# Optimization experiments

Measured on AMD Instinct MI355X. Metric: run time of the kernel, lower is better.

Reference implementation:

```python
import jax, jax.numpy as jnp
import numpy as np

N = 50000
E = 1600000
IN_DIM = 128
H = 8
D = 16  # out_dim per head


def setup_inputs() -> dict:
    key = jax.random.key(0)
    ks = jax.random.split(key, 9)
    h = jax.random.normal(ks[0], (N, IN_DIM), dtype=jnp.float32)
    src = jax.random.randint(ks[1], (E,), 0, N, dtype=jnp.int32)
    dst = jax.random.randint(ks[2], (E,), 0, N, dtype=jnp.int32)
    s = 1.0 / np.sqrt(IN_DIM)
    WQ = jax.random.uniform(ks[3], (IN_DIM, H * D), jnp.float32, -s, s)
    WK = jax.random.uniform(ks[4], (IN_DIM, H * D), jnp.float32, -s, s)
    WV = jax.random.uniform(ks[5], (IN_DIM, H * D), jnp.float32, -s, s)
    bQ = jax.random.uniform(ks[6], (H * D,), jnp.float32, -s, s)
    bK = jax.random.uniform(ks[7], (H * D,), jnp.float32, -s, s)
    bV = jax.random.uniform(ks[8], (H * D,), jnp.float32, -s, s)
    return {"h": h, "src": src, "dst": dst, "WQ": WQ, "WK": WK, "WV": WV,
            "bQ": bQ, "bK": bK, "bV": bV}


def reference(h, src, dst, WQ, WK, WV, bQ, bK, bV):
    # Node projections -> [N, H, D]
    Q = (h @ WQ + bQ).reshape(-1, H, D)
    K = (h @ WK + bK).reshape(-1, H, D)
    V = (h @ WV + bV).reshape(-1, H, D)
    # Edge scores: dot(K[src], Q[dst]) per head, scaled+clamped exp -> [E, H]
    scale = jnp.float32(np.sqrt(D))
    score = jnp.exp(jnp.clip(jnp.sum(K[src] * Q[dst], axis=-1) / scale, -5.0, 5.0))
    # Scatter-sum to destination nodes
    wV = jax.ops.segment_sum(score[:, :, None] * V[src], dst, num_segments=N)  # [N, H, D]
    z = jax.ops.segment_sum(score, dst, num_segments=N)  # [N, H]
    return wV / z[:, :, None]
```

## Files before the change

kernel.cpp:

```cpp
#include <hip/hip_runtime.h>

#define N_NODES 50000
#define N_PAD   50048
#define N_EDGES 1600000
#define HD 128
#define CHUNK 2048
#define NCHUNK ((N_EDGES + CHUNK - 1) / CHUNK)
#define NBUCKET ((N_NODES + 127) / 128)

typedef __attribute__((ext_vector_type(8))) short short8;
typedef __attribute__((ext_vector_type(4))) float floatx4;

union U4S8 { uint4 u; short8 s; };

__device__ __forceinline__ unsigned short f2bf(float f) {
    unsigned u = __float_as_uint(f);
    unsigned r = (u + 0x7fffu + ((u >> 16) & 1u)) >> 16;
    return (unsigned short)r;
}

#define HB_BLOCKS ((N_PAD * HD / 8) / 256)

__global__ __launch_bounds__(256) void prep_kernel(
    const float* __restrict__ h,
    const float* __restrict__ WQ, const float* __restrict__ WK, const float* __restrict__ WV,
    unsigned short* __restrict__ hb, unsigned short* __restrict__ Wf) {
    int bid = blockIdx.x, t = threadIdx.x;
    if (bid < HB_BLOCKS) {
        int tid = bid * 256 + t;
        int row = tid >> 4, c8 = tid & 15;
        uint4 outv;
        if (row < N_NODES) {
            const float4* src = (const float4*)(h + (size_t)row * HD + c8 * 8);
            float4 a = src[0], b = src[1];
            unsigned short r[8];
            r[0] = f2bf(a.x); r[1] = f2bf(a.y);
            r[2] = f2bf(a.z); r[3] = f2bf(a.w);
            r[4] = f2bf(b.x); r[5] = f2bf(b.y);
            r[6] = f2bf(b.z); r[7] = f2bf(b.w);
            outv = *(uint4*)r;
        } else {
            outv = make_uint4(0, 0, 0, 0);
        }
        *(uint4*)(hb + (size_t)tid * 8) = outv;
    } else {
        int tid = (bid - HB_BLOCKS) * 256 + t;
        if (tid < 24 * 4 * 64) {
            int lane = tid & 63;
            int kstep = (tid >> 6) & 3;
            int ntile = tid >> 8;
            int g = ntile >> 3;
            int c = (ntile & 7) * 16 + (lane & 15);
            int k0 = kstep * 32 + (lane >> 4) * 8;
            const float* W = (g == 0) ? WQ : (g == 1) ? WK : WV;
            unsigned short r[8];
#pragma unroll
            for (int j = 0; j < 8; ++j)
                r[j] = f2bf(W[(size_t)(k0 + j) * HD + c]);
            *(uint4*)(Wf + (size_t)tid * 8) = *(uint4*)r;
        }
    }
}


__global__ __launch_bounds__(256) void k_chunkhist(const int* __restrict__ dst,
                                                   int* __restrict__ chunkhist,
                                                   int* __restrict__ btot) {
    __shared__ int hist[NBUCKET];
    int t = threadIdx.x, c = blockIdx.x;
    for (int i = t; i < NBUCKET; i += 256) hist[i] = 0;
    __syncthreads();
    int e0 = c * CHUNK;
    int cnt = min(CHUNK, N_EDGES - e0);
    for (int i = t; i < cnt; i += 256)
        atomicAdd(&hist[dst[e0 + i] >> 7], 1);
    __syncthreads();
    for (int i = t; i < NBUCKET; i += 256) {
        int v = hist[i];
        chunkhist[c * NBUCKET + i] = v;
        if (v) atomicAdd(&btot[i], v);
    }
}

__global__ __launch_bounds__(512) void k_bscan(const int* __restrict__ btot,
                                               int* __restrict__ bucket_ptr) {
    int t = threadIdx.x;
    int v = (t < NBUCKET) ? btot[t] : 0;
    __shared__ int part[512];
    part[t] = v;
    __syncthreads();
    for (int off = 1; off < 512; off <<= 1) {
        int x = (t >= off) ? part[t - off] : 0;
        __syncthreads();
        part[t] += x;
        __syncthreads();
    }
    if (t < NBUCKET) bucket_ptr[t] = part[t] - v;
    if (t == NBUCKET - 1) bucket_ptr[NBUCKET] = part[t];
}

__global__ __launch_bounds__(256) void k_choff(const int* __restrict__ chunkhist,
                                               const int* __restrict__ bucket_ptr,
                                               int* __restrict__ chunkoff) {
    const int PER = (NCHUNK + 255) / 256;
    int b = blockIdx.x, t = threadIdx.x;
    int c0 = t * PER;
    int v[PER];
    int s = 0;
#pragma unroll
    for (int i = 0; i < PER; ++i) {
        int c = c0 + i;
        v[i] = (c < NCHUNK) ? chunkhist[c * NBUCKET + b] : 0;
        s += v[i];
    }
    __shared__ int part[256];
    part[t] = s;
    __syncthreads();
    for (int off = 1; off < 256; off <<= 1) {
        int x = (t >= off) ? part[t - off] : 0;
        __syncthreads();
        part[t] += x;
        __syncthreads();
    }
    int run = bucket_ptr[b] + part[t] - s;
#pragma unroll
    for (int i = 0; i < PER; ++i) {
        int c = c0 + i;
        if (c < NCHUNK) { chunkoff[c * NBUCKET + b] = run; run += v[i]; }
    }
}

__global__ __launch_bounds__(256) void k_scatter(const int* __restrict__ src,
                                                 const int* __restrict__ dst,
                                                 const int* __restrict__ chunkoff,
                                                 int* __restrict__ packed) {
    __shared__ int cur[NBUCKET];
    int t = threadIdx.x, c = blockIdx.x;
    for (int i = t; i < NBUCKET; i += 256) cur[i] = chunkoff[c * NBUCKET + i];
    __syncthreads();
    int e0 = c * CHUNK;
    int cnt = min(CHUNK, N_EDGES - e0);
    for (int i = t; i < cnt; i += 256) {
        int d = dst[e0 + i], s = src[e0 + i];
        int pos = atomicAdd(&cur[d >> 7], 1);
        packed[pos] = (s << 7) | (d & 127);
    }
}

__global__ __launch_bounds__(256) void k_finalize(const int* __restrict__ bucket_ptr,
                                                  const int* __restrict__ packed,
                                                  int* __restrict__ row_ptr,
                                                  int* __restrict__ col_src) {
    __shared__ int hist[128], part[128], cur[128];
    int b = blockIdx.x, t = threadIdx.x;
    if (t < 128) hist[t] = 0;
    __syncthreads();
    int ebeg = bucket_ptr[b], eend = bucket_ptr[b + 1];
    int m = eend - ebeg;
    for (int i = t; i < m; i += 256)
        atomicAdd(&hist[packed[ebeg + i] & 127], 1);
    __syncthreads();
    int v = 0;
    if (t < 128) { v = hist[t]; part[t] = v; }
    __syncthreads();
    for (int off = 1; off < 128; off <<= 1) {
        int x = 0;
        if (t < 128 && t >= off) x = part[t - off];
        __syncthreads();
        if (t < 128) part[t] += x;
        __syncthreads();
    }
    if (t < 128) {
        int excl = part[t] - v;
        int node = b * 128 + t;
        if (node < N_NODES) row_ptr[node] = ebeg + excl;
        if (node == N_NODES - 1) row_ptr[N_NODES] = eend;
        cur[t] = ebeg + excl;
    }
    __syncthreads();
    for (int i = t; i < m; i += 256) {
        int p = packed[ebeg + i];
        int pos = atomicAdd(&cur[p & 127], 1);
        col_src[pos] = p >> 7;
    }
}


__global__ __launch_bounds__(256) void proj_mfma(
    const unsigned short* __restrict__ hb, const unsigned short* __restrict__ Wf,
    const float* __restrict__ bQ, const float* __restrict__ bK, const float* __restrict__ bV,
    float* __restrict__ Qo, unsigned short* __restrict__ Kb, unsigned short* __restrict__ Vb) {
    int t = threadIdx.x;
    int w = t >> 6;
    int l = t & 63;
    int m0 = blockIdx.x * 64;
    int nt0 = w * 6;

    floatx4 acc[4][6];
#pragma unroll
    for (int mt = 0; mt < 4; ++mt)
#pragma unroll
        for (int nt = 0; nt < 6; ++nt)
            acc[mt][nt] = (floatx4){0.f, 0.f, 0.f, 0.f};

    int arow = m0 + (l & 15);
    int akoff = (l >> 4) * 8;

#pragma unroll
    for (int kstep = 0; kstep < 4; ++kstep) {
        short8 a[4], b[6];
#pragma unroll
        for (int mt = 0; mt < 4; ++mt) {
            U4S8 u;
            u.u = *(const uint4*)(hb + (size_t)(arow + mt * 16) * HD + akoff + kstep * 32);
            a[mt] = u.s;
        }
#pragma unroll
        for (int nt = 0; nt < 6; ++nt) {
            U4S8 u;
            u.u = *(const uint4*)(Wf + ((size_t)((nt0 + nt) * 4 + kstep) * 64 + l) * 8);
            b[nt] = u.s;
        }
#pragma unroll
        for (int mt = 0; mt < 4; ++mt)
#pragma unroll
            for (int nt = 0; nt < 6; ++nt)
                acc[mt][nt] = __builtin_amdgcn_mfma_f32_16x16x32_bf16(
                    a[mt], b[nt], acc[mt][nt], 0, 0, 0);
    }

#pragma unroll
    for (int nt = 0; nt < 6; ++nt) {
        int ntile = nt0 + nt;
        int g = ntile >> 3;
        int cc = (ntile & 7) * 16 + (l & 15);
        float bias = (g == 0) ? bQ[cc] : (g == 1) ? bK[cc] : bV[cc];
#pragma unroll
        for (int mt = 0; mt < 4; ++mt) {
#pragma unroll
            for (int r = 0; r < 4; ++r) {
                int grow = m0 + mt * 16 + (l >> 4) * 4 + r;
                if (grow < N_NODES) {
                    float val = acc[mt][nt][r] + bias;
                    if (g == 0)      Qo[(size_t)grow * HD + cc] = val;
                    else if (g == 1) Kb[(size_t)grow * HD + cc] = f2bf(val);
                    else             Vb[(size_t)grow * HD + cc] = f2bf(val);
                }
            }
        }
    }
}


__device__ __forceinline__ float blo(unsigned u) { return __uint_as_float(u << 16); }
__device__ __forceinline__ float bhi(unsigned u) { return __uint_as_float(u & 0xffff0000u); }

__global__ __launch_bounds__(64) void attn_kernel(
    const float* __restrict__ Q,
    const unsigned short* __restrict__ Kb, const unsigned short* __restrict__ Vb,
    const int* __restrict__ row_ptr, const int* __restrict__ col_src,
    float* __restrict__ out) {
    int n = blockIdx.x;
    int t = threadIdx.x;
    int o = t >> 3;
    int p = t & 7;

    const float4* Qv = (const float4*)(Q + (size_t)n * HD + p * 16);
    float4 q0 = Qv[0], q1 = Qv[1], q2 = Qv[2], q3 = Qv[3];

    float acc[16];
#pragma unroll
    for (int j = 0; j < 16; ++j) acc[j] = 0.f;
    float z = 0.f;

    int beg = row_ptr[n], end = row_ptr[n + 1];

    for (int base = beg; base < end; base += 64) {
        int mm = min(64, end - base);
        int e_l = col_src[(base + t < end) ? (base + t) : beg];
        int steps = (mm + 7) >> 3;

        int s0 = __shfl(e_l, o);
        const uint4* Kp = (const uint4*)(Kb + (size_t)s0 * HD + p * 16);
        const uint4* Vp = (const uint4*)(Vb + (size_t)s0 * HD + p * 16);
        uint4 ka = Kp[0], kb = Kp[1], va = Vp[0], vb = Vp[1];

        for (int i = 0; i < steps; ++i) {
            uint4 nka = ka, nkb = kb, nva = va, nvb = vb;
            if (i + 1 < steps) {
                int s1 = __shfl(e_l, 8 * (i + 1) + o);
                const uint4* Kn = (const uint4*)(Kb + (size_t)s1 * HD + p * 16);
                const uint4* Vn = (const uint4*)(Vb + (size_t)s1 * HD + p * 16);
                nka = Kn[0]; nkb = Kn[1]; nva = Vn[0]; nvb = Vn[1];
            }
            float dot = blo(ka.x) * q0.x + bhi(ka.x) * q0.y
                      + blo(ka.y) * q0.z + bhi(ka.y) * q0.w
                      + blo(ka.z) * q1.x + bhi(ka.z) * q1.y
                      + blo(ka.w) * q1.z + bhi(ka.w) * q1.w
                      + blo(kb.x) * q2.x + bhi(kb.x) * q2.y
                      + blo(kb.y) * q2.z + bhi(kb.y) * q2.w
                      + blo(kb.z) * q3.x + bhi(kb.z) * q3.y
                      + blo(kb.w) * q3.z + bhi(kb.w) * q3.w;
            float sc = __expf(fminf(fmaxf(dot * 0.25f, -5.f), 5.f));
            if (8 * i + o >= mm) sc = 0.f;
            acc[0]  = fmaf(sc, blo(va.x), acc[0]);
            acc[1]  = fmaf(sc, bhi(va.x), acc[1]);
            acc[2]  = fmaf(sc, blo(va.y), acc[2]);
            acc[3]  = fmaf(sc, bhi(va.y), acc[3]);
            acc[4]  = fmaf(sc, blo(va.z), acc[4]);
            acc[5]  = fmaf(sc, bhi(va.z), acc[5]);
            acc[6]  = fmaf(sc, blo(va.w), acc[6]);
            acc[7]  = fmaf(sc, bhi(va.w), acc[7]);
            acc[8]  = fmaf(sc, blo(vb.x), acc[8]);
            acc[9]  = fmaf(sc, bhi(vb.x), acc[9]);
            acc[10] = fmaf(sc, blo(vb.y), acc[10]);
            acc[11] = fmaf(sc, bhi(vb.y), acc[11]);
            acc[12] = fmaf(sc, blo(vb.z), acc[12]);
            acc[13] = fmaf(sc, bhi(vb.z), acc[13]);
            acc[14] = fmaf(sc, blo(vb.w), acc[14]);
            acc[15] = fmaf(sc, bhi(vb.w), acc[15]);
            z += sc;
            ka = nka; kb = nkb; va = nva; vb = nvb;
        }
    }

#pragma unroll
    for (int j = 0; j < 16; ++j) {
        acc[j] += __shfl_xor(acc[j], 8);
        acc[j] += __shfl_xor(acc[j], 16);
        acc[j] += __shfl_xor(acc[j], 32);
    }
    z += __shfl_xor(z, 8);
    z += __shfl_xor(z, 16);
    z += __shfl_xor(z, 32);

    if (o == 0) {
        float inv = 1.f / z;
        float4* O = (float4*)(out + (size_t)n * HD + p * 16);
        O[0] = (float4){acc[0] * inv,  acc[1] * inv,  acc[2] * inv,  acc[3] * inv};
        O[1] = (float4){acc[4] * inv,  acc[5] * inv,  acc[6] * inv,  acc[7] * inv};
        O[2] = (float4){acc[8] * inv,  acc[9] * inv,  acc[10] * inv, acc[11] * inv};
        O[3] = (float4){acc[12] * inv, acc[13] * inv, acc[14] * inv, acc[15] * inv};
    }
}


static inline char* align256(char* p) {
    return (char*)(((uintptr_t)p + 255) & ~(uintptr_t)255);
}

extern "C" void kernel_launch(void* const* d_in, const int* in_sizes, int n_in,
                              void* d_out, int out_size, void* d_ws, size_t ws_size,
                              hipStream_t stream) {
    const float* h  = (const float*)d_in[0];
    const int*   src = (const int*)d_in[1];
    const int*   dst = (const int*)d_in[2];
    const float* WQ = (const float*)d_in[3];
    const float* WK = (const float*)d_in[4];
    const float* WV = (const float*)d_in[5];
    const float* bQ = (const float*)d_in[6];
    const float* bK = (const float*)d_in[7];
    const float* bV = (const float*)d_in[8];
    float* out = (float*)d_out;

    char* p = (char*)d_ws;
    float* Q = (float*)p;                 p += (size_t)N_PAD * HD * 4;
    unsigned short* Kb = (unsigned short*)p; p += (size_t)N_PAD * HD * 2;
    unsigned short* Vb = (unsigned short*)p; p += (size_t)N_PAD * HD * 2;
    unsigned short* hb = (unsigned short*)p; p += (size_t)N_PAD * HD * 2;
    unsigned short* Wf = (unsigned short*)p; p += (size_t)24 * 4 * 64 * 8 * 2;
    p = align256(p);
    int* row_ptr    = (int*)p;            p += (N_NODES + 2) * 4;
    p = align256(p);
    int* bucket_ptr = (int*)p;            p += (NBUCKET + 1) * 4;
    p = align256(p);
    int* btot       = (int*)p;            p += NBUCKET * 4;
    p = align256(p);
    int* chunkhist  = (int*)p;            p += (size_t)NCHUNK * NBUCKET * 4;
    p = align256(p);
    int* chunkoff   = (int*)p;            p += (size_t)NCHUNK * NBUCKET * 4;
    p = align256(p);
    int* packed     = (int*)p;            p += (size_t)N_EDGES * 4;
    p = align256(p);
    int* col_src    = (int*)p;            p += (size_t)N_EDGES * 4;

    (void)hipMemsetAsync(btot, 0, NBUCKET * sizeof(int), stream);
    prep_kernel<<<HB_BLOCKS + 24, 256, 0, stream>>>(h, WQ, WK, WV, hb, Wf);
    k_chunkhist<<<NCHUNK, 256, 0, stream>>>(dst, chunkhist, btot);
    k_bscan<<<1, 512, 0, stream>>>(btot, bucket_ptr);
    k_choff<<<NBUCKET, 256, 0, stream>>>(chunkhist, bucket_ptr, chunkoff);
    k_scatter<<<NCHUNK, 256, 0, stream>>>(src, dst, chunkoff, packed);
    k_finalize<<<NBUCKET, 256, 0, stream>>>(bucket_ptr, packed, row_ptr, col_src);
    proj_mfma<<<N_PAD / 64, 256, 0, stream>>>(hb, Wf, bQ, bK, bV, Q, Kb, Vb);
    attn_kernel<<<N_NODES, 64, 0, stream>>>(Q, Kb, Vb, row_ptr, col_src, out);
}
```

Before: 307.0 us.

## Fuse bf16 conversion into projection, merge scan kernels, vectorize edge sorting

```diff
diff --git a/kernel.cpp b/kernel.cpp
--- a/kernel.cpp
+++ b/kernel.cpp
@@ -4,7 +4,7 @@
 #define N_PAD   50048
 #define N_EDGES 1600000
 #define HD 128
-#define CHUNK 2048
+#define CHUNK 4096
 #define NCHUNK ((N_EDGES + CHUNK - 1) / CHUNK)
 #define NBUCKET ((N_NODES + 127) / 128)
 
@@ -19,46 +19,27 @@
     return (unsigned short)r;
 }
 
-#define HB_BLOCKS ((N_PAD * HD / 8) / 256)
-
 __global__ __launch_bounds__(256) void prep_kernel(
-    const float* __restrict__ h,
     const float* __restrict__ WQ, const float* __restrict__ WK, const float* __restrict__ WV,
-    unsigned short* __restrict__ hb, unsigned short* __restrict__ Wf) {
+    unsigned short* __restrict__ Wf, int* __restrict__ btot) {
     int bid = blockIdx.x, t = threadIdx.x;
-    if (bid < HB_BLOCKS) {
+    if (bid < 24) {
         int tid = bid * 256 + t;
-        int row = tid >> 4, c8 = tid & 15;
-        uint4 outv;
-        if (row < N_NODES) {
-            const float4* src = (const float4*)(h + (size_t)row * HD + c8 * 8);
-            float4 a = src[0], b = src[1];
-            unsigned short r[8];
-            r[0] = f2bf(a.x); r[1] = f2bf(a.y);
-            r[2] = f2bf(a.z); r[3] = f2bf(a.w);
-            r[4] = f2bf(b.x); r[5] = f2bf(b.y);
-            r[6] = f2bf(b.z); r[7] = f2bf(b.w);
-            outv = *(uint4*)r;
-        } else {
-            outv = make_uint4(0, 0, 0, 0);
-        }
-        *(uint4*)(hb + (size_t)tid * 8) = outv;
+        int lane = tid & 63;
+        int kstep = (tid >> 6) & 3;
+        int ntile = tid >> 8;
+        int g = ntile >> 3;
+        int c = (ntile & 7) * 16 + (lane & 15);
+        int k0 = kstep * 32 + (lane >> 4) * 8;
+        const float* W = (g == 0) ? WQ : (g == 1) ? WK : WV;
+        unsigned short r[8];
+#pragma unroll
+        for (int j = 0; j < 8; ++j)
+            r[j] = f2bf(W[(size_t)(k0 + j) * HD + c]);
+        *(uint4*)(Wf + (size_t)tid * 8) = *(uint4*)r;
     } else {
-        int tid = (bid - HB_BLOCKS) * 256 + t;
-        if (tid < 24 * 4 * 64) {
-            int lane = tid & 63;
-            int kstep = (tid >> 6) & 3;
-            int ntile = tid >> 8;
-            int g = ntile >> 3;
-            int c = (ntile & 7) * 16 + (lane & 15);
-            int k0 = kstep * 32 + (lane >> 4) * 8;
-            const float* W = (g == 0) ? WQ : (g == 1) ? WK : WV;
-            unsigned short r[8];
-#pragma unroll
-            for (int j = 0; j < 8; ++j)
-                r[j] = f2bf(W[(size_t)(k0 + j) * HD + c]);
-            *(uint4*)(Wf + (size_t)tid * 8) = *(uint4*)r;
-        }
+        int i = (bid - 24) * 256 + t;
+        if (i < NBUCKET) btot[i] = 0;
     }
 }
 
@@ -72,8 +53,15 @@
     __syncthreads();
     int e0 = c * CHUNK;
     int cnt = min(CHUNK, N_EDGES - e0);
-    for (int i = t; i < cnt; i += 256)
-        atomicAdd(&hist[dst[e0 + i] >> 7], 1);
+    const uint4* d4 = (const uint4*)(dst + e0);
+    int cnt4 = cnt >> 2;
+    for (int i = t; i < cnt4; i += 256) {
+        uint4 v = d4[i];
+        atomicAdd(&hist[v.x >> 7], 1);
+        atomicAdd(&hist[v.y >> 7], 1);
+        atomicAdd(&hist[v.z >> 7], 1);
+        atomicAdd(&hist[v.w >> 7], 1);
+    }
     __syncthreads();
     for (int i = t; i < NBUCKET; i += 256) {
         int v = hist[i];
@@ -82,28 +70,27 @@
     }
 }
 
-__global__ __launch_bounds__(512) void k_bscan(const int* __restrict__ btot,
-                                               int* __restrict__ bucket_ptr) {
-    int t = threadIdx.x;
-    int v = (t < NBUCKET) ? btot[t] : 0;
-    __shared__ int part[512];
-    part[t] = v;
-    __syncthreads();
-    for (int off = 1; off < 512; off <<= 1) {
-        int x = (t >= off) ? part[t - off] : 0;
-        __syncthreads();
-        part[t] += x;
-        __syncthreads();
-    }
-    if (t < NBUCKET) bucket_ptr[t] = part[t] - v;
-    if (t == NBUCKET - 1) bucket_ptr[NBUCKET] = part[t];
-}
-
 __global__ __launch_bounds__(256) void k_choff(const int* __restrict__ chunkhist,
-                                               const int* __restrict__ bucket_ptr,
+                                               const int* __restrict__ btot,
+                                               int* __restrict__ bucket_ptr,
                                                int* __restrict__ chunkoff) {
+    int b = blockIdx.x, t = threadIdx.x;
+    int x = 0;
+    for (int i = t; i < NBUCKET; i += 256)
+        if (i < b) x += btot[i];
+    __shared__ int red[256];
+    red[t] = x;
+    __syncthreads();
+    for (int off = 128; off > 0; off >>= 1) {
+        if (t < off) red[t] += red[t + off];
+        __syncthreads();
+    }
+    int base = red[0];
+    if (t == 0) {
+        bucket_ptr[b] = base;
+        if (b == NBUCKET - 1) bucket_ptr[NBUCKET] = base + btot[b];
+    }
     const int PER = (NCHUNK + 255) / 256;
-    int b = blockIdx.x, t = threadIdx.x;
     int c0 = t * PER;
     int v[PER];
     int s = 0;
@@ -117,12 +104,12 @@
     part[t] = s;
     __syncthreads();
     for (int off = 1; off < 256; off <<= 1) {
-        int x = (t >= off) ? part[t - off] : 0;
-        __syncthreads();
-        part[t] += x;
-        __syncthreads();
-    }
-    int run = bucket_ptr[b] + part[t] - s;
+        int y = (t >= off) ? part[t - off] : 0;
+        __syncthreads();
+        part[t] += y;
+        __syncthreads();
+    }
+    int run = base + part[t] - s;
 #pragma unroll
     for (int i = 0; i < PER; ++i) {
         int c = c0 + i;
@@ -140,10 +127,17 @@
     __syncthreads();
     int e0 = c * CHUNK;
     int cnt = min(CHUNK, N_EDGES - e0);
-    for (int i = t; i < cnt; i += 256) {
-        int d = dst[e0 + i], s = src[e0 + i];
-        int pos = atomicAdd(&cur[d >> 7], 1);
-        packed[pos] = (s << 7) | (d & 127);
+    const uint4* d4 = (const uint4*)(dst + e0);
+    const uint4* s4 = (const uint4*)(src + e0);
+    int cnt4 = cnt >> 2;
+    for (int i = t; i < cnt4; i += 256) {
+        uint4 d = d4[i];
+        uint4 s = s4[i];
+        int pos;
+        pos = atomicAdd(&cur[d.x >> 7], 1); packed[pos] = (s.x << 7) | (d.x & 127);
+        pos = atomicAdd(&cur[d.y >> 7], 1); packed[pos] = (s.y << 7) | (d.y & 127);
+        pos = atomicAdd(&cur[d.z >> 7], 1); packed[pos] = (s.z << 7) | (d.z & 127);
+        pos = atomicAdd(&cur[d.w >> 7], 1); packed[pos] = (s.w << 7) | (d.w & 127);
     }
 }
 
@@ -187,7 +181,7 @@
 
 
 __global__ __launch_bounds__(256) void proj_mfma(
-    const unsigned short* __restrict__ hb, const unsigned short* __restrict__ Wf,
+    const float* __restrict__ h, const unsigned short* __restrict__ Wf,
     const float* __restrict__ bQ, const float* __restrict__ bK, const float* __restrict__ bV,
     float* __restrict__ Qo, unsigned short* __restrict__ Kb, unsigned short* __restrict__ Vb) {
     int t = threadIdx.x;
@@ -211,9 +205,18 @@
         short8 a[4], b[6];
 #pragma unroll
         for (int mt = 0; mt < 4; ++mt) {
-            U4S8 u;
-            u.u = *(const uint4*)(hb + (size_t)(arow + mt * 16) * HD + akoff + kstep * 32);
-            a[mt] = u.s;
+            int row = arow + mt * 16;
+            unsigned short r[8];
+            if (row < N_NODES) {
+                const float4* ap = (const float4*)(h + (size_t)row * HD + akoff + kstep * 32);
+                float4 f0 = ap[0], f1 = ap[1];
+                r[0] = f2bf(f0.x); r[1] = f2bf(f0.y); r[2] = f2bf(f0.z); r[3] = f2bf(f0.w);
+                r[4] = f2bf(f1.x); r[5] = f2bf(f1.y); r[6] = f2bf(f1.z); r[7] = f2bf(f1.w);
+            } else {
+#pragma unroll
+                for (int j = 0; j < 8; ++j) r[j] = 0;
+            }
+            a[mt] = *(short8*)r;
         }
 #pragma unroll
         for (int nt = 0; nt < 6; ++nt) {
@@ -255,15 +258,16 @@
 __device__ __forceinline__ float blo(unsigned u) { return __uint_as_float(u << 16); }
 __device__ __forceinline__ float bhi(unsigned u) { return __uint_as_float(u & 0xffff0000u); }
 
-__global__ __launch_bounds__(64) void attn_kernel(
+__global__ __launch_bounds__(256) void attn_kernel(
     const float* __restrict__ Q,
     const unsigned short* __restrict__ Kb, const unsigned short* __restrict__ Vb,
     const int* __restrict__ row_ptr, const int* __restrict__ col_src,
     float* __restrict__ out) {
-    int n = blockIdx.x;
-    int t = threadIdx.x;
-    int o = t >> 3;
-    int p = t & 7;
+    int n = blockIdx.x * 4 + (threadIdx.x >> 6);
+    if (n >= N_NODES) return;
+    int l = threadIdx.x & 63;
+    int o = l >> 3;
+    int p = l & 7;
 
     const float4* Qv = (const float4*)(Q + (size_t)n * HD + p * 16);
     float4 q0 = Qv[0], q1 = Qv[1], q2 = Qv[2], q3 = Qv[3];
@@ -277,7 +281,7 @@
 
     for (int base = beg; base < end; base += 64) {
         int mm = min(64, end - base);
-        int e_l = col_src[(base + t < end) ? (base + t) : beg];
+        int e_l = col_src[(base + l < end) ? (base + l) : beg];
         int steps = (mm + 7) >> 3;
 
         int s0 = __shfl(e_l, o);
@@ -364,33 +368,30 @@
     float* out = (float*)d_out;
 
     char* p = (char*)d_ws;
-    float* Q = (float*)p;                 p += (size_t)N_PAD * HD * 4;
+    float* Q = (float*)p;                    p += (size_t)N_PAD * HD * 4;
     unsigned short* Kb = (unsigned short*)p; p += (size_t)N_PAD * HD * 2;
     unsigned short* Vb = (unsigned short*)p; p += (size_t)N_PAD * HD * 2;
-    unsigned short* hb = (unsigned short*)p; p += (size_t)N_PAD * HD * 2;
     unsigned short* Wf = (unsigned short*)p; p += (size_t)24 * 4 * 64 * 8 * 2;
     p = align256(p);
-    int* row_ptr    = (int*)p;            p += (N_NODES + 2) * 4;
-    p = align256(p);
-    int* bucket_ptr = (int*)p;            p += (NBUCKET + 1) * 4;
-    p = align256(p);
-    int* btot       = (int*)p;            p += NBUCKET * 4;
-    p = align256(p);
-    int* chunkhist  = (int*)p;            p += (size_t)NCHUNK * NBUCKET * 4;
-    p = align256(p);
-    int* chunkoff   = (int*)p;            p += (size_t)NCHUNK * NBUCKET * 4;
-    p = align256(p);
-    int* packed     = (int*)p;            p += (size_t)N_EDGES * 4;
-    p = align256(p);
-    int* col_src    = (int*)p;            p += (size_t)N_EDGES * 4;
-
-    (void)hipMemsetAsync(btot, 0, NBUCKET * sizeof(int), stream);
-    prep_kernel<<<HB_BLOCKS + 24, 256, 0, stream>>>(h, WQ, WK, WV, hb, Wf);
+    int* row_ptr    = (int*)p;               p += (N_NODES + 2) * 4;
+    p = align256(p);
+    int* bucket_ptr = (int*)p;               p += (NBUCKET + 1) * 4;
+    p = align256(p);
+    int* btot       = (int*)p;               p += NBUCKET * 4;
+    p = align256(p);
+    int* chunkhist  = (int*)p;               p += (size_t)NCHUNK * NBUCKET * 4;
+    p = align256(p);
+    int* chunkoff   = (int*)p;               p += (size_t)NCHUNK * NBUCKET * 4;
+    p = align256(p);
+    int* packed     = (int*)p;               p += (size_t)N_EDGES * 4;
+    p = align256(p);
+    int* col_src    = (int*)p;               p += (size_t)N_EDGES * 4;
+
+    prep_kernel<<<26, 256, 0, stream>>>(WQ, WK, WV, Wf, btot);
     k_chunkhist<<<NCHUNK, 256, 0, stream>>>(dst, chunkhist, btot);
-    k_bscan<<<1, 512, 0, stream>>>(btot, bucket_ptr);
-    k_choff<<<NBUCKET, 256, 0, stream>>>(chunkhist, bucket_ptr, chunkoff);
+    k_choff<<<NBUCKET, 256, 0, stream>>>(chunkhist, btot, bucket_ptr, chunkoff);
     k_scatter<<<NCHUNK, 256, 0, stream>>>(src, dst, chunkoff, packed);
     k_finalize<<<NBUCKET, 256, 0, stream>>>(bucket_ptr, packed, row_ptr, col_src);
-    proj_mfma<<<N_PAD / 64, 256, 0, stream>>>(hb, Wf, bQ, bK, bV, Q, Kb, Vb);
-    attn_kernel<<<N_NODES, 64, 0, stream>>>(Q, Kb, Vb, row_ptr, col_src, out);
-}
+    proj_mfma<<<N_PAD / 64, 256, 0, stream>>>(h, Wf, bQ, bK, bV, Q, Kb, Vb);
+    attn_kernel<<<(N_NODES + 3) / 4, 256, 0, stream>>>(Q, Kb, Vb, row_ptr, col_src, out);
+}
```

Measured after the change: 292.7 us. 1.05x faster.
